# Kernel optimization log

Hardware: AMD Instinct MI355X
Metric: run time of the kernel (lower is better)

Reference implementation:

```python
import jax, jax.numpy as jnp
import numpy as np

B, IN, H = 8192, 1024, 1024

def _ln(x, g, b, eps=1e-5):
    mu = jnp.mean(x, axis=-1, keepdims=True)
    var = jnp.mean(jnp.square(x - mu), axis=-1, keepdims=True)
    return (x - mu) * jax.lax.rsqrt(var + eps) * g + b

def setup_inputs() -> dict:
    key = jax.random.key(0)
    ks = jax.random.split(key, 8)
    s_h = 1.0 / np.sqrt(H)
    s_i = 1.0 / np.sqrt(IN)
    inp = {
        'x': jax.random.normal(ks[0], (B, IN), jnp.float32),
        'h': jax.random.normal(ks[1], (B, H), jnp.float32),
        'W_r': jax.random.uniform(ks[2], (H, H), jnp.float32, -s_h, s_h),
        'U_r': jax.random.uniform(ks[3], (H, IN), jnp.float32, -s_i, s_i),
        'W_u': jax.random.uniform(ks[4], (H, H), jnp.float32, -s_h, s_h),
        'U_u': jax.random.uniform(ks[5], (H, IN), jnp.float32, -s_i, s_i),
        'W_c': jax.random.uniform(ks[6], (H, H), jnp.float32, -s_h, s_h),
        'U_c': jax.random.uniform(ks[7], (H, IN), jnp.float32, -s_i, s_i),
        # LayerNorm params: rows = [r_hidden, r_input, u_hidden, u_input, c_hidden, c_input]
        'ln_gamma': 0.1 * jnp.ones((6, H), jnp.float32),
        'ln_beta': jnp.zeros((6, H), jnp.float32),
    }
    return inp

def reference(x, h, W_r, U_r, W_u, U_u, W_c, U_c, ln_gamma, ln_beta):
    g, b = ln_gamma, ln_beta
    # nn.Linear(bias=False): y = x @ W.T
    r = jax.nn.sigmoid(_ln(h @ W_r.T, g[0], b[0]) + _ln(x @ U_r.T, g[1], b[1]))
    u = jax.nn.sigmoid(_ln(h @ W_u.T, g[2], b[2]) + _ln(x @ U_u.T, g[3], b[3]))
    c = jnp.tanh(_ln((h * r) @ W_c.T, g[4], b[4]) + _ln(x @ U_c.T, g[5], b[5]))
    return (1.0 - u) * h + u * c
```

## Files before the change

kernel.cpp:

```cpp
#include <hip/hip_runtime.h>
#include <cstdint>
#include <cstddef>

typedef unsigned short u16;
typedef __attribute__((ext_vector_type(8))) short bf16x8;
typedef __attribute__((ext_vector_type(4))) float f32x4;

__device__ inline float bf2f(u16 u) { return __uint_as_float(((unsigned)u) << 16); }
__device__ inline u16 f2bf(float f) {
  unsigned u = __float_as_uint(f);
  u += 0x7fffu + ((u >> 16) & 1u);
  return (u16)(u >> 16);
}

__device__ inline void async16(const u16* g, u16* l) {
  __builtin_amdgcn_global_load_lds(
      (const __attribute__((address_space(1))) void*)g,
      (__attribute__((address_space(3))) void*)l, 16, 0, 0);
}

__device__ inline void unpack8(uint4 q, float* o) {
  o[0] = bf2f((u16)(q.x & 0xffffu)); o[1] = bf2f((u16)(q.x >> 16));
  o[2] = bf2f((u16)(q.y & 0xffffu)); o[3] = bf2f((u16)(q.y >> 16));
  o[4] = bf2f((u16)(q.z & 0xffffu)); o[5] = bf2f((u16)(q.z >> 16));
  o[6] = bf2f((u16)(q.w & 0xffffu)); o[7] = bf2f((u16)(q.w >> 16));
}

__device__ inline uint4 pack8(const float* v) {
  uint4 q;
  q.x = (unsigned)f2bf(v[0]) | ((unsigned)f2bf(v[1]) << 16);
  q.y = (unsigned)f2bf(v[2]) | ((unsigned)f2bf(v[3]) << 16);
  q.z = (unsigned)f2bf(v[4]) | ((unsigned)f2bf(v[5]) << 16);
  q.w = (unsigned)f2bf(v[6]) | ((unsigned)f2bf(v[7]) << 16);
  return q;
}

__device__ inline float fast_sigmoid(float z) {
  return 1.0f / (1.0f + exp2f(-1.4426950408889634f * z));
}
__device__ inline float fast_tanh(float z) {
  return 1.0f - 2.0f / (1.0f + exp2f(2.8853900817779268f * z));
}

struct ConvAll { const float* src[8]; u16* dst[8]; };

__global__ __launch_bounds__(256) void convert_all(ConvAll a) {
  const int b = blockIdx.x;
  int which, off;
  if (b < 8192)        { which = 0; off = b; }
  else if (b < 16384)  { which = 1; off = b - 8192; }
  else { const int t = b - 16384; which = 2 + (t >> 10); off = t & 1023; }
  const float* __restrict__ s = a.src[which];
  u16* __restrict__ d = a.dst[which];
  const int i = (off * 256 + threadIdx.x) * 4;
  float4 v = *(const float4*)(s + i);
  uint2 o;
  o.x = (unsigned)f2bf(v.x) | ((unsigned)f2bf(v.y) << 16);
  o.y = (unsigned)f2bf(v.z) | ((unsigned)f2bf(v.w) << 16);
  *(uint2*)(d + i) = o;
}

struct Gemm4 { const u16* A[4]; const u16* Bw[4]; u16* Y[4]; };

template <int NG_LOG2>
__global__ __launch_bounds__(256) void gemm_batch(Gemm4 args) {
  const int p = blockIdx.x;
  const int xcd = p & 7;
  const int s = p >> 3;
  const int pr = s >> (3 + NG_LOG2);
  const int cc = s & ((8 << NG_LOG2) - 1);
  const int gate = cc >> 3;
  const int col  = cc & 7;
  const int r = pr * 8 + xcd;

  const u16* __restrict__ A  = args.A[gate];
  const u16* __restrict__ Bw = args.Bw[gate];
  u16* __restrict__ Y = args.Y[gate];

  __shared__ __attribute__((aligned(16))) u16 As[128 * 64];
  __shared__ __attribute__((aligned(16))) u16 Bs[128 * 64];

  const int tid  = threadIdx.x;
  const int lane = tid & 63;
  const int w    = tid >> 6;
  const int wm   = w >> 1;
  const int wn   = w & 1;

  const int rowBlk = r * 128;
  const int colBlk = col * 128;

  const int srow = lane >> 3;
  const int scol = ((lane & 7) ^ srow) * 8;
  const u16* gA[4]; const u16* gB[4]; u16* lA[4]; u16* lB[4];
#pragma unroll
  for (int i = 0; i < 4; i++) {
    const int rr = w * 32 + i * 8;
    gA[i] = A  + (size_t)(rowBlk + rr + srow) * 1024 + scol;
    gB[i] = Bw + (size_t)(colBlk + rr + srow) * 1024 + scol;
    lA[i] = &As[rr * 64];
    lB[i] = &Bs[rr * 64];
  }

  const int swz = (((lane >> 4) ^ (lane & 7)) << 3);
  const int fa = (wm * 64 + (lane & 15)) * 64 + swz;
  const int fb = (wn * 64 + (lane & 15)) * 64 + swz;

  f32x4 acc[4][4] = {};

  for (int k0 = 0; k0 < 1024; k0 += 64) {
#pragma unroll
    for (int i = 0; i < 4; i++) {
      async16(gA[i] + k0, lA[i]);
      async16(gB[i] + k0, lB[i]);
    }
    __syncthreads();
#pragma unroll
    for (int kk = 0; kk < 2; kk++) {
      const int kx = kk << 5;
      bf16x8 af[4], bfr[4];
#pragma unroll
      for (int t = 0; t < 4; t++) {
        af[t]  = *(const bf16x8*)&As[(fa + t * 1024) ^ kx];
        bfr[t] = *(const bf16x8*)&Bs[(fb + t * 1024) ^ kx];
      }
#pragma unroll
      for (int tm = 0; tm < 4; tm++)
#pragma unroll
        for (int tn = 0; tn < 4; tn++)
          acc[tm][tn] = __builtin_amdgcn_mfma_f32_16x16x32_bf16(af[tm], bfr[tn], acc[tm][tn], 0, 0, 0);
    }
    __syncthreads();
  }

  const int rBase = rowBlk + wm * 64 + (lane >> 4) * 4;
  const int cBase = colBlk + wn * 64 + (lane & 15);
#pragma unroll
  for (int tm = 0; tm < 4; tm++) {
#pragma unroll
    for (int i = 0; i < 4; i++) {
      const size_t rr = (size_t)(rBase + tm * 16 + i);
#pragma unroll
      for (int tn = 0; tn < 4; tn++)
        Y[rr * 1024 + cBase + tn * 16] = f2bf(acc[tm][tn][i]);
    }
  }
}

__global__ __launch_bounds__(256) void rgate_kernel(
    const u16* __restrict__ Yrh, const u16* __restrict__ Yrx,
    const u16* __restrict__ hb, const float* __restrict__ gamma,
    const float* __restrict__ beta, u16* __restrict__ hrb) {
  const int row  = blockIdx.x * 4 + (threadIdx.x >> 6);
  const int lane = threadIdx.x & 63;
  const size_t rb = (size_t)row * 1024;

  uint4 qa[2], qb[2], qh[2];
  qa[0] = *(const uint4*)(Yrh + rb + lane * 8);
  qa[1] = *(const uint4*)(Yrh + rb + 512 + lane * 8);
  qb[0] = *(const uint4*)(Yrx + rb + lane * 8);
  qb[1] = *(const uint4*)(Yrx + rb + 512 + lane * 8);
  qh[0] = *(const uint4*)(hb  + rb + lane * 8);
  qh[1] = *(const uint4*)(hb  + rb + 512 + lane * 8);

  float s0 = 0.f, s0q = 0.f, s1 = 0.f, s1q = 0.f;
  float tmp[8];
#pragma unroll
  for (int c = 0; c < 2; c++) {
    unpack8(qa[c], tmp);
#pragma unroll
    for (int j = 0; j < 8; j++) { s0 += tmp[j]; s0q += tmp[j] * tmp[j]; }
    unpack8(qb[c], tmp);
#pragma unroll
    for (int j = 0; j < 8; j++) { s1 += tmp[j]; s1q += tmp[j] * tmp[j]; }
  }
#pragma unroll
  for (int off = 1; off < 64; off <<= 1) {
    s0 += __shfl_xor(s0, off, 64);  s0q += __shfl_xor(s0q, off, 64);
    s1 += __shfl_xor(s1, off, 64);  s1q += __shfl_xor(s1q, off, 64);
  }

  const float inv = 1.0f / 1024.0f;
  const float mu0 = s0 * inv, rs0 = rsqrtf(s0q * inv - mu0 * mu0 + 1e-5f);
  const float mu1 = s1 * inv, rs1 = rsqrtf(s1q * inv - mu1 * mu1 + 1e-5f);

#pragma unroll
  for (int c = 0; c < 2; c++) {
    const int cb = c * 512 + lane * 8;
    float va[8], vb[8], vh[8], o[8];
    unpack8(qa[c], va); unpack8(qb[c], vb); unpack8(qh[c], vh);
#pragma unroll
    for (int j = 0; j < 8; j++) {
      const float ln0 = (va[j] - mu0) * rs0 * gamma[cb + j] + beta[cb + j];
      const float ln1 = (vb[j] - mu1) * rs1 * gamma[1024 + cb + j] + beta[1024 + cb + j];
      const float rg = fast_sigmoid(ln0 + ln1);
      o[j] = vh[j] * rg;
    }
    *(uint4*)(hrb + rb + cb) = pack8(o);
  }
}

__global__ __launch_bounds__(256) void final_fuse(
    const u16* __restrict__ Yuh, const u16* __restrict__ Yux,
    const u16* __restrict__ Ych, const u16* __restrict__ Ycx,
    const float* __restrict__ h, const float* __restrict__ gamma,
    const float* __restrict__ beta, float* __restrict__ out) {
  const int row  = blockIdx.x * 4 + (threadIdx.x >> 6);
  const int lane = threadIdx.x & 63;
  const size_t rb = (size_t)row * 1024;

  uint4 q0[2], q1[2], q2[2], q3[2];
  float4 hf[4];
#pragma unroll
  for (int c = 0; c < 2; c++) {
    const int cb = c * 512 + lane * 8;
    q0[c] = *(const uint4*)(Yuh + rb + cb);
    q1[c] = *(const uint4*)(Yux + rb + cb);
    q2[c] = *(const uint4*)(Ych + rb + cb);
    q3[c] = *(const uint4*)(Ycx + rb + cb);
    hf[c * 2]     = *(const float4*)(h + rb + cb);
    hf[c * 2 + 1] = *(const float4*)(h + rb + cb + 4);
  }

  float s[8] = {0.f, 0.f, 0.f, 0.f, 0.f, 0.f, 0.f, 0.f};
  float tmp[8];
#pragma unroll
  for (int c = 0; c < 2; c++) {
    unpack8(q0[c], tmp);
#pragma unroll
    for (int j = 0; j < 8; j++) { s[0] += tmp[j]; s[1] += tmp[j] * tmp[j]; }
    unpack8(q1[c], tmp);
#pragma unroll
    for (int j = 0; j < 8; j++) { s[2] += tmp[j]; s[3] += tmp[j] * tmp[j]; }
    unpack8(q2[c], tmp);
#pragma unroll
    for (int j = 0; j < 8; j++) { s[4] += tmp[j]; s[5] += tmp[j] * tmp[j]; }
    unpack8(q3[c], tmp);
#pragma unroll
    for (int j = 0; j < 8; j++) { s[6] += tmp[j]; s[7] += tmp[j] * tmp[j]; }
  }
#pragma unroll
  for (int off = 1; off < 64; off <<= 1) {
#pragma unroll
    for (int q = 0; q < 8; q++) s[q] += __shfl_xor(s[q], off, 64);
  }

  const float inv = 1.0f / 1024.0f;
  const float mu0 = s[0] * inv, rs0 = rsqrtf(s[1] * inv - mu0 * mu0 + 1e-5f);
  const float mu1 = s[2] * inv, rs1 = rsqrtf(s[3] * inv - mu1 * mu1 + 1e-5f);
  const float mu2 = s[4] * inv, rs2 = rsqrtf(s[5] * inv - mu2 * mu2 + 1e-5f);
  const float mu3 = s[6] * inv, rs3 = rsqrtf(s[7] * inv - mu3 * mu3 + 1e-5f);

#pragma unroll
  for (int c = 0; c < 2; c++) {
    const int cb = c * 512 + lane * 8;
    float v0[8], v1[8], v2[8], v3[8];
    unpack8(q0[c], v0); unpack8(q1[c], v1); unpack8(q2[c], v2); unpack8(q3[c], v3);
    const float* hv = (const float*)&hf[c * 2];
    float o[8];
#pragma unroll
    for (int j = 0; j < 8; j++) {
      const int cc = cb + j;
      const float ln2 = (v0[j] - mu0) * rs0 * gamma[2 * 1024 + cc] + beta[2 * 1024 + cc];
      const float ln3 = (v1[j] - mu1) * rs1 * gamma[3 * 1024 + cc] + beta[3 * 1024 + cc];
      const float ln4 = (v2[j] - mu2) * rs2 * gamma[4 * 1024 + cc] + beta[4 * 1024 + cc];
      const float ln5 = (v3[j] - mu3) * rs3 * gamma[5 * 1024 + cc] + beta[5 * 1024 + cc];
      const float u  = fast_sigmoid(ln2 + ln3);
      const float cg = fast_tanh(ln4 + ln5);
      o[j] = (1.0f - u) * hv[j] + u * cg;
    }
    *(float4*)(out + rb + cb)     = *(float4*)&o[0];
    *(float4*)(out + rb + cb + 4) = *(float4*)&o[4];
  }
}

extern "C" void kernel_launch(void* const* d_in, const int* in_sizes, int n_in,
                              void* d_out, int out_size, void* d_ws, size_t ws_size,
                              hipStream_t stream) {
  const float* x  = (const float*)d_in[0];
  const float* h  = (const float*)d_in[1];
  const float* Ws[6] = {(const float*)d_in[2], (const float*)d_in[3],
                        (const float*)d_in[4], (const float*)d_in[5],
                        (const float*)d_in[6], (const float*)d_in[7]};
  const float* gamma = (const float*)d_in[8];
  const float* beta  = (const float*)d_in[9];
  float* out = (float*)d_out;

  char* ws = (char*)d_ws;
  const size_t SZ_ACT = (size_t)8192 * 1024 * 2;
  const size_t SZ_W   = (size_t)1024 * 1024 * 2;

  u16* xb = (u16*)(ws);
  u16* hb = (u16*)(ws + SZ_ACT);
  u16* wb[6];
  for (int i = 0; i < 6; i++) wb[i] = (u16*)(ws + 2 * SZ_ACT + i * SZ_W);
  char* ybase = ws + 2 * SZ_ACT + 6 * SZ_W;
  u16* Y0 = (u16*)(ybase);
  u16* Y1 = (u16*)(ybase + SZ_ACT);
  u16* Y2 = (u16*)(ybase + 2 * SZ_ACT);
  u16* Y3 = (u16*)(ybase + 3 * SZ_ACT);
  u16* Y5 = (u16*)(ybase + 4 * SZ_ACT);

  ConvAll ca = {};
  ca.src[0] = x; ca.dst[0] = xb;
  ca.src[1] = h; ca.dst[1] = hb;
  for (int i = 0; i < 6; i++) { ca.src[2 + i] = Ws[i]; ca.dst[2 + i] = wb[i]; }
  convert_all<<<16384 + 6 * 1024, 256, 0, stream>>>(ca);

  Gemm4 ga = {};
  ga.A[0] = hb; ga.Bw[0] = wb[0]; ga.Y[0] = Y0;
  ga.A[1] = xb; ga.Bw[1] = wb[1]; ga.Y[1] = Y1;
  gemm_batch<1><<<1024, 256, 0, stream>>>(ga);

  rgate_kernel<<<2048, 256, 0, stream>>>(Y0, Y1, hb, gamma, beta, Y1);

  Gemm4 gb = {};
  gb.A[0] = xb; gb.Bw[0] = wb[3]; gb.Y[0] = Y3;
  gb.A[1] = xb; gb.Bw[1] = wb[5]; gb.Y[1] = Y5;
  gb.A[2] = hb; gb.Bw[2] = wb[2]; gb.Y[2] = Y2;
  gb.A[3] = Y1; gb.Bw[3] = wb[4]; gb.Y[3] = Y0;
  gemm_batch<2><<<2048, 256, 0, stream>>>(gb);

  final_fuse<<<2048, 256, 0, stream>>>(Y2, Y3, Y0, Y5, h, gamma, beta, out);
}
```

Measured before the change: 299.2 us.

## Compute the r-gate GEMMs in FP8 with scaled MFMA instructions

Converts x, h, W_r and U_r to FP8 E4M3, applying a power-of-two prescale to the weights, and runs the two r-gate GEMMs with the 16x16x128 scaled FP8 MFMA. Loading half the bytes per element and using the higher-throughput MFMA is meant to cut the cost of the first GEMM stage. In exchange the convert pass does extra work, writing both bf16 and fp8 copies of the activations. The reset gate loses precision, although LayerNorm followed by a sigmoid may tolerate this.

```diff
diff --git a/kernel.cpp b/kernel.cpp
--- a/kernel.cpp
+++ b/kernel.cpp
@@ -3,20 +3,44 @@
 #include <cstddef>
 
 typedef unsigned short u16;
+typedef unsigned char u8;
 typedef __attribute__((ext_vector_type(8))) short bf16x8;
 typedef __attribute__((ext_vector_type(4))) float f32x4;
+typedef __attribute__((ext_vector_type(4))) int i32x4;
+typedef __attribute__((ext_vector_type(8))) int i32x8;
 
 __device__ inline float bf2f(u16 u) { return __uint_as_float(((unsigned)u) << 16); }
-__device__ inline u16 f2bf(float f) {
+__device__ inline unsigned f2bf(float f) {
   unsigned u = __float_as_uint(f);
   u += 0x7fffu + ((u >> 16) & 1u);
-  return (u16)(u >> 16);
-}
-
-__device__ inline void async16(const u16* g, u16* l) {
+  return u >> 16;
+}
+
+__device__ inline unsigned f2fp8(float f) {
+  unsigned s = (__float_as_uint(f) >> 31) << 7;
+  float a = fabsf(f);
+  if (a >= 0.015625f) {
+    unsigned u = __float_as_uint(a);
+    u += 0x7FFFFu + ((u >> 20) & 1u);
+    unsigned e = (u >> 23) - 120u;
+    unsigned m = (u >> 20) & 7u;
+    return s | (e << 3) | m;
+  }
+  int m = (int)rintf(a * 512.0f);
+  return s | (unsigned)m;
+}
+
+__device__ inline void async16(const void* g, void* l) {
   __builtin_amdgcn_global_load_lds(
       (const __attribute__((address_space(1))) void*)g,
       (__attribute__((address_space(3))) void*)l, 16, 0, 0);
+}
+
+__device__ inline i32x8 join8(i32x4 lo, i32x4 hi) {
+  i32x8 r;
+  r[0] = lo[0]; r[1] = lo[1]; r[2] = lo[2]; r[3] = lo[3];
+  r[4] = hi[0]; r[5] = hi[1]; r[6] = hi[2]; r[7] = hi[3];
+  return r;
 }
 
 __device__ inline void unpack8(uint4 q, float* o) {
@@ -28,10 +52,10 @@
 
 __device__ inline uint4 pack8(const float* v) {
   uint4 q;
-  q.x = (unsigned)f2bf(v[0]) | ((unsigned)f2bf(v[1]) << 16);
-  q.y = (unsigned)f2bf(v[2]) | ((unsigned)f2bf(v[3]) << 16);
-  q.z = (unsigned)f2bf(v[4]) | ((unsigned)f2bf(v[5]) << 16);
-  q.w = (unsigned)f2bf(v[6]) | ((unsigned)f2bf(v[7]) << 16);
+  q.x = f2bf(v[0]) | (f2bf(v[1]) << 16);
+  q.y = f2bf(v[2]) | (f2bf(v[3]) << 16);
+  q.z = f2bf(v[4]) | (f2bf(v[5]) << 16);
+  q.w = f2bf(v[6]) | (f2bf(v[7]) << 16);
   return q;
 }
 
@@ -42,22 +66,143 @@
   return 1.0f - 2.0f / (1.0f + exp2f(2.8853900817779268f * z));
 }
 
-struct ConvAll { const float* src[8]; u16* dst[8]; };
-
-__global__ __launch_bounds__(256) void convert_all(ConvAll a) {
+struct ConvArgs2 {
+  const float* x; const float* h; const float* wr; const float* ur;
+  const float* wbf[4];
+  u16* xb; u16* hb; u8* x8; u8* h8; u8* w8r; u8* w8u;
+  u16* wbo[4];
+};
+
+__global__ __launch_bounds__(256) void convert_all(ConvArgs2 a) {
   const int b = blockIdx.x;
-  int which, off;
-  if (b < 8192)        { which = 0; off = b; }
-  else if (b < 16384)  { which = 1; off = b - 8192; }
-  else { const int t = b - 16384; which = 2 + (t >> 10); off = t & 1023; }
-  const float* __restrict__ s = a.src[which];
-  u16* __restrict__ d = a.dst[which];
-  const int i = (off * 256 + threadIdx.x) * 4;
-  float4 v = *(const float4*)(s + i);
-  uint2 o;
-  o.x = (unsigned)f2bf(v.x) | ((unsigned)f2bf(v.y) << 16);
-  o.y = (unsigned)f2bf(v.z) | ((unsigned)f2bf(v.w) << 16);
-  *(uint2*)(d + i) = o;
+  const int t = threadIdx.x;
+  if (b < 16384) {
+    const bool isx = b < 8192;
+    const int off = isx ? b : b - 8192;
+    const float* __restrict__ s = isx ? a.x : a.h;
+    u16* __restrict__ db = isx ? a.xb : a.hb;
+    u8*  __restrict__ d8 = isx ? a.x8 : a.h8;
+    const int i = (off * 256 + t) * 4;
+    float4 v = *(const float4*)(s + i);
+    uint2 o;
+    o.x = f2bf(v.x) | (f2bf(v.y) << 16);
+    o.y = f2bf(v.z) | (f2bf(v.w) << 16);
+    *(uint2*)(db + i) = o;
+    unsigned q = f2fp8(v.x) | (f2fp8(v.y) << 8) | (f2fp8(v.z) << 16) | (f2fp8(v.w) << 24);
+    *(unsigned*)(d8 + i) = q;
+  } else if (b < 18432) {
+    const bool isr = b < 17408;
+    const int off = isr ? b - 16384 : b - 17408;
+    const float* __restrict__ s = isr ? a.wr : a.ur;
+    u8* __restrict__ d8 = isr ? a.w8r : a.w8u;
+    const int i = (off * 256 + t) * 4;
+    float4 v = *(const float4*)(s + i);
+    unsigned q = f2fp8(v.x * 8192.f) | (f2fp8(v.y * 8192.f) << 8) |
+                 (f2fp8(v.z * 8192.f) << 16) | (f2fp8(v.w * 8192.f) << 24);
+    *(unsigned*)(d8 + i) = q;
+  } else {
+    const int tt = b - 18432;
+    const int which = tt >> 10;
+    const int off = tt & 1023;
+    const float* __restrict__ s = a.wbf[which];
+    u16* __restrict__ d = a.wbo[which];
+    const int i = (off * 256 + t) * 4;
+    float4 v = *(const float4*)(s + i);
+    uint2 o;
+    o.x = f2bf(v.x) | (f2bf(v.y) << 16);
+    o.y = f2bf(v.z) | (f2bf(v.w) << 16);
+    *(uint2*)(d + i) = o;
+  }
+}
+
+struct GemmF8 { const u8* A[2]; const u8* Bw[2]; u16* Y[2]; };
+
+__global__ __launch_bounds__(256) void gemm_fp8(GemmF8 args) {
+  const int p = blockIdx.x;
+  const int xcd = p & 7;
+  const int s = p >> 3;
+  const int pr = s >> 4;
+  const int cc = s & 15;
+  const int gate = cc >> 3;
+  const int col = cc & 7;
+  const int r = pr * 8 + xcd;
+
+  const u8* __restrict__ A  = args.A[gate];
+  const u8* __restrict__ Bw = args.Bw[gate];
+  u16* __restrict__ Y = args.Y[gate];
+
+  __shared__ __attribute__((aligned(16))) u8 As[128 * 128];
+  __shared__ __attribute__((aligned(16))) u8 Bs[128 * 128];
+
+  const int tid  = threadIdx.x;
+  const int lane = tid & 63;
+  const int w    = tid >> 6;
+  const int wm   = w >> 1;
+  const int wn   = w & 1;
+
+  const int rowBlk = r * 128;
+  const int colBlk = col * 128;
+
+  const int srow = lane >> 3;
+  const int scol = ((lane & 7) ^ srow) * 16;
+  const u8* gA[4]; const u8* gB[4]; u8* lA[4]; u8* lB[4];
+#pragma unroll
+  for (int i = 0; i < 4; i++) {
+    const int rr = w * 32 + i * 8;
+    gA[i] = A  + (size_t)(rowBlk + rr + srow) * 1024 + scol;
+    gB[i] = Bw + (size_t)(colBlk + rr + srow) * 1024 + scol;
+    lA[i] = &As[rr * 128];
+    lB[i] = &Bs[rr * 128];
+  }
+
+  const int sw = lane & 7;
+  const int g0 = (lane >> 4) * 2;
+  const int o0 = ((g0 ^ sw) << 4);
+  const int o1 = (((g0 + 1) ^ sw) << 4);
+  const int frA = (wm * 64 + (lane & 15)) * 128;
+  const int frB = (wn * 64 + (lane & 15)) * 128;
+
+  f32x4 acc[4][4] = {};
+
+  for (int k0 = 0; k0 < 1024; k0 += 128) {
+#pragma unroll
+    for (int i = 0; i < 4; i++) {
+      async16(gA[i] + k0, lA[i]);
+      async16(gB[i] + k0, lB[i]);
+    }
+    __syncthreads();
+    i32x8 af[4], bfr[4];
+#pragma unroll
+    for (int t = 0; t < 4; t++) {
+      const int ra = frA + t * 16 * 128;
+      const int rb = frB + t * 16 * 128;
+      af[t]  = join8(*(const i32x4*)&As[ra + o0], *(const i32x4*)&As[ra + o1]);
+      bfr[t] = join8(*(const i32x4*)&Bs[rb + o0], *(const i32x4*)&Bs[rb + o1]);
+    }
+#pragma unroll
+    for (int tm = 0; tm < 4; tm++)
+#pragma unroll
+      for (int tn = 0; tn < 4; tn++)
+        acc[tm][tn] = __builtin_amdgcn_mfma_scale_f32_16x16x128_f8f6f4(
+            af[tm], bfr[tn], acc[tm][tn],
+            0, 0,
+            0, 127,
+            0, 114);
+    __syncthreads();
+  }
+
+  const int rBase = rowBlk + wm * 64 + (lane >> 4) * 4;
+  const int cBase = colBlk + wn * 64 + (lane & 15);
+#pragma unroll
+  for (int tm = 0; tm < 4; tm++) {
+#pragma unroll
+    for (int i = 0; i < 4; i++) {
+      const size_t rr = (size_t)(rBase + tm * 16 + i);
+#pragma unroll
+      for (int tn = 0; tn < 4; tn++)
+        Y[rr * 1024 + cBase + tn * 16] = (u16)f2bf(acc[tm][tn][i]);
+    }
+  }
 }
 
 struct Gemm4 { const u16* A[4]; const u16* Bw[4]; u16* Y[4]; };
@@ -141,7 +286,7 @@
       const size_t rr = (size_t)(rBase + tm * 16 + i);
 #pragma unroll
       for (int tn = 0; tn < 4; tn++)
-        Y[rr * 1024 + cBase + tn * 16] = f2bf(acc[tm][tn][i]);
+        Y[rr * 1024 + cBase + tn * 16] = (u16)f2bf(acc[tm][tn][i]);
     }
   }
 }
@@ -278,46 +423,55 @@
                               hipStream_t stream) {
   const float* x  = (const float*)d_in[0];
   const float* h  = (const float*)d_in[1];
-  const float* Ws[6] = {(const float*)d_in[2], (const float*)d_in[3],
-                        (const float*)d_in[4], (const float*)d_in[5],
-                        (const float*)d_in[6], (const float*)d_in[7]};
+  const float* W_r = (const float*)d_in[2];
+  const float* U_r = (const float*)d_in[3];
+  const float* W_u = (const float*)d_in[4];
+  const float* U_u = (const float*)d_in[5];
+  const float* W_c = (const float*)d_in[6];
+  const float* U_c = (const float*)d_in[7];
   const float* gamma = (const float*)d_in[8];
   const float* beta  = (const float*)d_in[9];
   float* out = (float*)d_out;
 
   char* ws = (char*)d_ws;
-  const size_t SZ_ACT = (size_t)8192 * 1024 * 2;
-  const size_t SZ_W   = (size_t)1024 * 1024 * 2;
+  const size_t MB = 1024 * 1024;
+  const size_t SZ_ACT = 16 * MB;
 
   u16* xb = (u16*)(ws);
-  u16* hb = (u16*)(ws + SZ_ACT);
-  u16* wb[6];
-  for (int i = 0; i < 6; i++) wb[i] = (u16*)(ws + 2 * SZ_ACT + i * SZ_W);
-  char* ybase = ws + 2 * SZ_ACT + 6 * SZ_W;
+  u16* hb = (u16*)(ws + 16 * MB);
+  u16* wb[4];
+  for (int i = 0; i < 4; i++) wb[i] = (u16*)(ws + (32 + 2 * i) * MB);
+  u8* w8r = (u8*)(ws + 40 * MB);
+  u8* w8u = (u8*)(ws + 41 * MB);
+  char* ybase = ws + 42 * MB;
   u16* Y0 = (u16*)(ybase);
   u16* Y1 = (u16*)(ybase + SZ_ACT);
   u16* Y2 = (u16*)(ybase + 2 * SZ_ACT);
   u16* Y3 = (u16*)(ybase + 3 * SZ_ACT);
   u16* Y5 = (u16*)(ybase + 4 * SZ_ACT);
-
-  ConvAll ca = {};
-  ca.src[0] = x; ca.dst[0] = xb;
-  ca.src[1] = h; ca.dst[1] = hb;
-  for (int i = 0; i < 6; i++) { ca.src[2 + i] = Ws[i]; ca.dst[2 + i] = wb[i]; }
-  convert_all<<<16384 + 6 * 1024, 256, 0, stream>>>(ca);
-
-  Gemm4 ga = {};
-  ga.A[0] = hb; ga.Bw[0] = wb[0]; ga.Y[0] = Y0;
-  ga.A[1] = xb; ga.Bw[1] = wb[1]; ga.Y[1] = Y1;
-  gemm_batch<1><<<1024, 256, 0, stream>>>(ga);
+  u8* x8 = (u8*)Y5;
+  u8* h8 = (u8*)Y5 + 8 * MB;
+
+  ConvArgs2 ca = {};
+  ca.x = x; ca.h = h; ca.wr = W_r; ca.ur = U_r;
+  ca.wbf[0] = W_u; ca.wbf[1] = U_u; ca.wbf[2] = W_c; ca.wbf[3] = U_c;
+  ca.xb = xb; ca.hb = hb; ca.x8 = x8; ca.h8 = h8; ca.w8r = w8r; ca.w8u = w8u;
+  ca.wbo[0] = (u16*)(ws + 32 * MB); ca.wbo[1] = (u16*)(ws + 34 * MB);
+  ca.wbo[2] = (u16*)(ws + 36 * MB); ca.wbo[3] = (u16*)(ws + 38 * MB);
+  convert_all<<<22528, 256, 0, stream>>>(ca);
+
+  GemmF8 gf = {};
+  gf.A[0] = h8; gf.Bw[0] = w8r; gf.Y[0] = Y0;
+  gf.A[1] = x8; gf.Bw[1] = w8u; gf.Y[1] = Y1;
+  gemm_fp8<<<1024, 256, 0, stream>>>(gf);
 
   rgate_kernel<<<2048, 256, 0, stream>>>(Y0, Y1, hb, gamma, beta, Y1);
 
   Gemm4 gb = {};
-  gb.A[0] = xb; gb.Bw[0] = wb[3]; gb.Y[0] = Y3;
-  gb.A[1] = xb; gb.Bw[1] = wb[5]; gb.Y[1] = Y5;
-  gb.A[2] = hb; gb.Bw[2] = wb[2]; gb.Y[2] = Y2;
-  gb.A[3] = Y1; gb.Bw[3] = wb[4]; gb.Y[3] = Y0;
+  gb.A[0] = xb; gb.Bw[0] = wb[1]; gb.Y[0] = Y3;
+  gb.A[1] = xb; gb.Bw[1] = wb[3]; gb.Y[1] = Y5;
+  gb.A[2] = hb; gb.Bw[2] = wb[0]; gb.Y[2] = Y2;
+  gb.A[3] = Y1; gb.Bw[3] = wb[2]; gb.Y[3] = Y0;
   gemm_batch<2><<<2048, 256, 0, stream>>>(gb);
 
   final_fuse<<<2048, 256, 0, stream>>>(Y2, Y3, Y0, Y5, h, gamma, beta, out);
```

Measured after the change: 284.8 us. 4.8% less time.
